# Performance work log

Hardware: AMD Instinct MI355X
Metric: run time of the kernel (lower is better)

The kernel has to match this reference:

```python
import jax, jax.numpy as jnp
import numpy as np

EPS = 1e-5
NEG_SLOPE = 0.01  # F.leaky_relu default


def setup_inputs() -> dict:
    key = jax.random.key(0)
    k1, k2, k3, k4 = jax.random.split(key, 4)
    N, F, H = 8192, 512, 2
    inputs = jax.random.normal(k1, (N, F), dtype=jnp.float32)
    adj = jnp.zeros((N, N), dtype=jnp.float32)  # accepted but unused by the module
    # torch Linear(F, F*H, bias=False): y = x @ W with W of shape [F, F*H]
    W = jax.random.normal(k2, (F, F * H), dtype=jnp.float32) * (1.0 / np.sqrt(F))
    a_w = jax.random.normal(k3, (1,), dtype=jnp.float32)  # Linear(1,1) weight
    a_b = jax.random.normal(k4, (1,), dtype=jnp.float32)  # Linear(1,1) bias
    return {"inputs": inputs, "adj": adj, "W": W, "a_w": a_w, "a_b": a_b}


def reference(inputs, adj, W, a_w, a_b):
    # Wh, Ws = chunk(inputs @ W, 2)
    WhWs = inputs @ W                       # [N, 2F]
    Wh, Ws = jnp.split(WhWs, 2, axis=-1)    # each [N, F]
    # bias = a(ones) = a_w * 1 + a_b  (constant scalar broadcast)
    bias = (a_w + a_b)[0]
    # dense attention: tanh(Wh + Ws + bias) @ Wh^T  -> [N, N]
    scores = jnp.tanh(Wh + Ws + bias) @ Wh.T
    attn = jax.nn.softmax(scores, axis=-1)  # [N, N]
    out = attn @ Wh + inputs                # [N, F] residual
    # training-mode batch norm over node dim, no affine
    mean = jnp.mean(out, axis=0)
    var = jnp.var(out, axis=0)
    out = (out - mean) * jax.lax.rsqrt(var + EPS)
    return jnp.where(out >= 0, out, NEG_SLOPE * out)
```

## Files before the change

### kernel.cpp

```cpp
#include <hip/hip_runtime.h>

using f32x4 = float    __attribute__((ext_vector_type(4)));
using f16x8 = _Float16 __attribute__((ext_vector_type(8)));

__device__ __forceinline__ void gload_lds16(const void* g, void* l) {
    __builtin_amdgcn_global_load_lds(
        (__attribute__((address_space(1))) void*)(void*)g,
        (__attribute__((address_space(3))) void*)l, 16, 0, 0);
}


__global__ __launch_bounds__(256) void k_cvt_x(
    const float* __restrict__ in, _Float16* __restrict__ out) {
    int i = (blockIdx.x * 256 + threadIdx.x) * 8;
    f32x4 a = *(const f32x4*)(in + i);
    f32x4 b = *(const f32x4*)(in + i + 4);
    f16x8 o;
    #pragma unroll
    for (int j = 0; j < 4; ++j) { o[j] = (_Float16)a[j]; o[j + 4] = (_Float16)b[j]; }
    *(f16x8*)(out + i) = o;
}

__global__ __launch_bounds__(256) void k_cvtT(
    const float* __restrict__ in, _Float16* __restrict__ out, int R, int C) {
    __shared__ _Float16 tile[32][33];
    int c0 = blockIdx.x * 32, r0 = blockIdx.y * 32;
    int tx = threadIdx.x & 31, ty = threadIdx.x >> 5;
    #pragma unroll
    for (int i = ty; i < 32; i += 8)
        tile[i][tx] = (_Float16)in[(size_t)(r0 + i) * C + c0 + tx];
    __syncthreads();
    #pragma unroll
    for (int i = ty; i < 32; i += 8)
        out[(size_t)(c0 + i) * R + r0 + tx] = tile[tx][i];
}

__global__ __launch_bounds__(256) void k_transpose16(
    const _Float16* __restrict__ in, _Float16* __restrict__ out, int R, int C) {
    __shared__ _Float16 tile[32][33];
    int c0 = blockIdx.x * 32, r0 = blockIdx.y * 32;
    int tx = threadIdx.x & 31, ty = threadIdx.x >> 5;
    #pragma unroll
    for (int i = ty; i < 32; i += 8)
        tile[i][tx] = in[(size_t)(r0 + i) * C + c0 + tx];
    __syncthreads();
    #pragma unroll
    for (int i = ty; i < 32; i += 8)
        out[(size_t)(c0 + i) * R + r0 + tx] = tile[tx][i];
}

template<int OM, int BN>
__global__ __launch_bounds__(256, 2) void k_gemm_bt(
    const _Float16* __restrict__ A, int lda,
    const _Float16* __restrict__ Bt, int ldb,
    void* __restrict__ Cp, int ldc, int K) {
    constexpr int BM  = 128;
    constexpr int NI  = BN / 32;
    constexpr int NCH = (BM + BN) / 16;
    __shared__ _Float16 As[BM * 32];
    __shared__ _Float16 Bs[BN * 32];
    const int row0 = blockIdx.y * BM, col0 = blockIdx.x * BN;
    const int tid = threadIdx.x, w = tid >> 6, lane = tid & 63;
    const int wm = w >> 1, wn = w & 1;
    const int lrow = lane & 15, quad = lane >> 4;
    const int r16 = lane >> 2;
    const int kc  = (((lane & 3) - ((lane >> 3) & 3)) & 3) * 8;
    const int sq  = ((quad + ((lrow >> 1) & 3)) & 3) * 8;
    f32x4 acc[4][NI] = {};

    for (int k0 = 0; k0 < K; k0 += 32) {
        #pragma unroll
        for (int i = 0; i < NCH / 4; ++i) {
            int c = w + i * 4;
            if (c < BM / 16) {
                gload_lds16(A + (size_t)(row0 + c * 16 + r16) * lda + (k0 + kc),
                            As + c * 512);
            } else {
                int c2 = c - BM / 16;
                gload_lds16(Bt + (size_t)(col0 + c2 * 16 + r16) * ldb + (k0 + kc),
                            Bs + c2 * 512);
            }
        }
        __syncthreads();
        f16x8 af[4], bfr[NI];
        #pragma unroll
        for (int i = 0; i < 4; ++i)
            af[i] = *(const f16x8*)(As + (wm * 64 + i * 16 + lrow) * 32 + sq);
        #pragma unroll
        for (int i = 0; i < NI; ++i)
            bfr[i] = *(const f16x8*)(Bs + (wn * (BN / 2) + i * 16 + lrow) * 32 + sq);
        #pragma unroll
        for (int mi = 0; mi < 4; ++mi)
            #pragma unroll
            for (int ni = 0; ni < NI; ++ni)
                acc[mi][ni] = __builtin_amdgcn_mfma_f32_16x16x32_f16(
                    af[mi], bfr[ni], acc[mi][ni], 0, 0, 0);
        __syncthreads();
    }
    #pragma unroll
    for (int mi = 0; mi < 4; ++mi) {
        #pragma unroll
        for (int ni = 0; ni < NI; ++ni) {
            int col = col0 + wn * (BN / 2) + ni * 16 + lrow;
            #pragma unroll
            for (int r = 0; r < 4; ++r) {
                int row = row0 + wm * 64 + mi * 16 + quad * 4 + r;
                float v = acc[mi][ni][r];
                if constexpr (OM == 1)
                    ((_Float16*)Cp)[(size_t)row * ldc + col] = (_Float16)v;
                else
                    ((float*)Cp)[(size_t)row * ldc + col] = v;
            }
        }
    }
}

__global__ __launch_bounds__(512, 4) void k_gemm3(
    const _Float16* __restrict__ A,
    const _Float16* __restrict__ Bt,
    float* __restrict__ Cp) {
    __shared__ _Float16 As[128 * 32];
    __shared__ _Float16 Bs[256 * 32];
    const int row0 = blockIdx.y * 128, col0 = blockIdx.x * 256;
    const size_t zoff = (size_t)blockIdx.z * 2048;
    Cp += (size_t)blockIdx.z * ((size_t)8192 * 512);
    const int tid = threadIdx.x, w = tid >> 6, lane = tid & 63;
    const int wm = w >> 2, wn = w & 3;
    const int lrow = lane & 15, quad = lane >> 4;
    const int r16 = lane >> 2;
    const int kc = (((lane & 3) - ((lane >> 3) & 3)) & 3) * 8;
    const int sq = ((quad + ((lrow >> 1) & 3)) & 3) * 8;
    f32x4 acc[4][4] = {};
    for (int k0 = 0; k0 < 2048; k0 += 32) {
        #pragma unroll
        for (int i = 0; i < 3; ++i) {
            int c = w + i * 8;
            if (c < 8) {
                gload_lds16(A + (size_t)(row0 + c * 16 + r16) * 8192 + zoff + k0 + kc,
                            As + c * 512);
            } else {
                int c2 = c - 8;
                gload_lds16(Bt + (size_t)(col0 + c2 * 16 + r16) * 8192 + zoff + k0 + kc,
                            Bs + c2 * 512);
            }
        }
        __syncthreads();
        f16x8 af[4], bf[4];
        #pragma unroll
        for (int i = 0; i < 4; ++i)
            af[i] = *(const f16x8*)(As + (wm * 64 + i * 16 + lrow) * 32 + sq);
        #pragma unroll
        for (int i = 0; i < 4; ++i)
            bf[i] = *(const f16x8*)(Bs + (wn * 64 + i * 16 + lrow) * 32 + sq);
        #pragma unroll
        for (int mi = 0; mi < 4; ++mi)
            #pragma unroll
            for (int ni = 0; ni < 4; ++ni)
                acc[mi][ni] = __builtin_amdgcn_mfma_f32_16x16x32_f16(
                    af[mi], bf[ni], acc[mi][ni], 0, 0, 0);
        __syncthreads();
    }
    #pragma unroll
    for (int mi = 0; mi < 4; ++mi) {
        #pragma unroll
        for (int ni = 0; ni < 4; ++ni) {
            int col = col0 + wn * 64 + ni * 16 + lrow;
            #pragma unroll
            for (int r = 0; r < 4; ++r) {
                int row = row0 + wm * 64 + mi * 16 + quad * 4 + r;
                Cp[(size_t)row * 512 + col] = acc[mi][ni][r];
            }
        }
    }
}

__global__ __launch_bounds__(256) void k_tanh_split(
    const float* __restrict__ WhWs, _Float16* __restrict__ T,
    _Float16* __restrict__ Wh,
    const float* __restrict__ aw, const float* __restrict__ ab) {
    int i = blockIdx.x * 256 + threadIdx.x;
    float bias = aw[0] + ab[0];
    int row = i >> 9, col = i & 511;
    float wh  = WhWs[(size_t)row * 1024 + col];
    float wsv = WhWs[(size_t)row * 1024 + 512 + col];
    Wh[i] = (_Float16)wh;
    T[i]  = (_Float16)tanhf(wh + wsv + bias);
}

__global__ __launch_bounds__(256) void k_softmax_rows(
    _Float16* __restrict__ S, int N) {
    const int row = blockIdx.x;
    _Float16* prow = S + (size_t)row * N;
    const int t = threadIdx.x;
    float v[32];
    #pragma unroll
    for (int it = 0; it < 4; ++it) {
        f16x8 h = *(const f16x8*)(prow + (it * 256 + t) * 8);
        #pragma unroll
        for (int j = 0; j < 8; ++j) v[it * 8 + j] = (float)h[j];
    }
    float m = v[0];
    #pragma unroll
    for (int j = 1; j < 32; ++j) m = fmaxf(m, v[j]);
    #pragma unroll
    for (int off = 32; off > 0; off >>= 1) m = fmaxf(m, __shfl_xor(m, off));
    __shared__ float red[8];
    const int wid = t >> 6, lane = t & 63;
    if (lane == 0) red[wid] = m;
    __syncthreads();
    m = fmaxf(fmaxf(red[0], red[1]), fmaxf(red[2], red[3]));
    float l = 0.f;
    #pragma unroll
    for (int j = 0; j < 32; ++j) l += __expf(v[j] - m);
    #pragma unroll
    for (int off = 32; off > 0; off >>= 1) l += __shfl_xor(l, off);
    if (lane == 0) red[4 + wid] = l;
    __syncthreads();
    float rl = 1.f / (red[4] + red[5] + red[6] + red[7]);
    #pragma unroll
    for (int it = 0; it < 4; ++it) {
        f16x8 pk;
        #pragma unroll
        for (int j = 0; j < 8; ++j)
            pk[j] = (_Float16)(__expf(v[it * 8 + j] - m) * rl);
        *(f16x8*)(prow + (it * 256 + t) * 8) = pk;
    }
}

__global__ __launch_bounds__(256) void k_reduce_stats(
    const float* __restrict__ part, const float* __restrict__ X,
    float* __restrict__ outf, float* __restrict__ cs, float* __restrict__ cq) {
    const int t = threadIdx.x;
    const int r0 = blockIdx.x * 32;
    constexpr size_t PS = (size_t)8192 * 512;
    float s0 = 0, q0 = 0, s1 = 0, q1 = 0;
    for (int r = 0; r < 32; ++r) {
        size_t base = (size_t)(r0 + r) * 512;
        float a = part[base + t] + part[PS + base + t]
                + part[2 * PS + base + t] + part[3 * PS + base + t] + X[base + t];
        float b = part[base + t + 256] + part[PS + base + t + 256]
                + part[2 * PS + base + t + 256] + part[3 * PS + base + t + 256]
                + X[base + t + 256];
        outf[base + t] = a;       outf[base + t + 256] = b;
        s0 += a; q0 += a * a; s1 += b; q1 += b * b;
    }
    atomicAdd(&cs[t], s0);       atomicAdd(&cq[t], q0);
    atomicAdd(&cs[t + 256], s1); atomicAdd(&cq[t + 256], q1);
}

__global__ __launch_bounds__(256) void k_bn_lrelu(
    const float* __restrict__ outf, const float* __restrict__ colsum,
    const float* __restrict__ colsq, float* __restrict__ out) {
    int i = blockIdx.x * 256 + threadIdx.x;
    int c = i & 511;
    constexpr float rN = 1.f / 8192.f;
    float mean = colsum[c] * rN;
    float var  = colsq[c] * rN - mean * mean;
    float y = (outf[i] - mean) * rsqrtf(var + 1e-5f);
    y = (y >= 0.f) ? y : 0.01f * y;
    out[i] = y;
}

extern "C" void kernel_launch(void* const* d_in, const int* in_sizes, int n_in,
                              void* d_out, int out_size, void* d_ws, size_t ws_size,
                              hipStream_t stream) {
    const float* X  = (const float*)d_in[0];
    const float* W  = (const float*)d_in[2];
    const float* aw = (const float*)d_in[3];
    const float* ab = (const float*)d_in[4];
    float* out = (float*)d_out;

    char* ws = (char*)d_ws;
    _Float16* Xh   = (_Float16*)(ws + 0x0);
    _Float16* Wt   = (_Float16*)(ws + 0x800000);
    float*    WhWs = (float*)   (ws + 0x900000);
    _Float16* T    = (_Float16*)(ws + 0x2900000);
    _Float16* Whh  = (_Float16*)(ws + 0x3100000);
    _Float16* WhT  = (_Float16*)(ws + 0x3900000);
    _Float16* S    = (_Float16*)(ws + 0x4100000);
    float*    outf = (float*)   (ws + 0xC100000);
    float*    part = (float*)   (ws + 0xD100000);
    float*    cs   = (float*)   (ws + 0x11100000);
    float*    cq   = (float*)   (ws + 0x11100800);

    hipMemsetAsync(cs, 0, 4096, stream);
    k_cvt_x<<<dim3((8192 * 512) / 2048), 256, 0, stream>>>(X, Xh);
    k_cvtT<<<dim3(1024 / 32, 512 / 32), 256, 0, stream>>>(W, Wt, 512, 1024);
    k_gemm_bt<0, 128><<<dim3(1024 / 128, 8192 / 128), 256, 0, stream>>>(
        Xh, 512, Wt, 512, WhWs, 1024, 512);
    k_tanh_split<<<dim3((8192 * 512) / 256), 256, 0, stream>>>(WhWs, T, Whh, aw, ab);
    k_transpose16<<<dim3(512 / 32, 8192 / 32), 256, 0, stream>>>(Whh, WhT, 8192, 512);
    k_gemm_bt<1, 128><<<dim3(8192 / 128, 8192 / 128), 256, 0, stream>>>(
        T, 512, Whh, 512, S, 8192, 512);
    k_softmax_rows<<<dim3(8192), 256, 0, stream>>>(S, 8192);
    k_gemm3<<<dim3(2, 64, 4), 512, 0, stream>>>(S, WhT, part);
    k_reduce_stats<<<dim3(256), 256, 0, stream>>>(part, X, outf, cs, cq);
    k_bn_lrelu<<<dim3((8192 * 512) / 256), 256, 0, stream>>>(outf, cs, cq, out);
}
```

Before: 565.8 us.

## Fuse tanh, split and transpose into first GEMM epilogue; enlarge score GEMM tile

The first GEMM now computes the matching Wh and Ws columns in the same block and applies tanh plus bias in its epilogue. It writes Wh, T and the transposed Wh directly, which removes the fp32 WhWs round trip, the tanh_split kernel and the transpose kernel. The score GEMM moves to a 256x128 tile with 512 threads, and softmax caches its exponentials instead of recomputing them. The risks are uncoalesced 8-byte strided stores to WhT and a different occupancy profile for the larger tile.

```diff
diff --git a/kernel.cpp b/kernel.cpp
--- a/kernel.cpp
+++ b/kernel.cpp
@@ -2,6 +2,7 @@
 
 using f32x4 = float    __attribute__((ext_vector_type(4)));
 using f16x8 = _Float16 __attribute__((ext_vector_type(8)));
+using f16x4 = _Float16 __attribute__((ext_vector_type(4)));
 
 __device__ __forceinline__ void gload_lds16(const void* g, void* l) {
     __builtin_amdgcn_global_load_lds(
@@ -35,81 +36,115 @@
         out[(size_t)(c0 + i) * R + r0 + tx] = tile[tx][i];
 }
 
-__global__ __launch_bounds__(256) void k_transpose16(
-    const _Float16* __restrict__ in, _Float16* __restrict__ out, int R, int C) {
-    __shared__ _Float16 tile[32][33];
-    int c0 = blockIdx.x * 32, r0 = blockIdx.y * 32;
-    int tx = threadIdx.x & 31, ty = threadIdx.x >> 5;
-    #pragma unroll
-    for (int i = ty; i < 32; i += 8)
-        tile[i][tx] = in[(size_t)(r0 + i) * C + c0 + tx];
-    __syncthreads();
-    #pragma unroll
-    for (int i = ty; i < 32; i += 8)
-        out[(size_t)(c0 + i) * R + r0 + tx] = tile[tx][i];
-}
-
-template<int OM, int BN>
-__global__ __launch_bounds__(256, 2) void k_gemm_bt(
-    const _Float16* __restrict__ A, int lda,
-    const _Float16* __restrict__ Bt, int ldb,
-    void* __restrict__ Cp, int ldc, int K) {
-    constexpr int BM  = 128;
-    constexpr int NI  = BN / 32;
-    constexpr int NCH = (BM + BN) / 16;
-    __shared__ _Float16 As[BM * 32];
-    __shared__ _Float16 Bs[BN * 32];
-    const int row0 = blockIdx.y * BM, col0 = blockIdx.x * BN;
+__global__ __launch_bounds__(512, 4) void k_gemm1f(
+    const _Float16* __restrict__ A, const _Float16* __restrict__ Bt,
+    _Float16* __restrict__ Whh, _Float16* __restrict__ T,
+    _Float16* __restrict__ WhT,
+    const float* __restrict__ aw, const float* __restrict__ ab) {
+    __shared__ _Float16 As[128 * 32];
+    __shared__ _Float16 B0s[64 * 32];
+    __shared__ _Float16 B1s[64 * 32];
+    const float bias = aw[0] + ab[0];
+    const int row0 = blockIdx.y * 128, col0 = blockIdx.x * 64;
+    const int tid = threadIdx.x, w = tid >> 6, lane = tid & 63;
+    const int wm = w >> 2, wn = w & 3;
+    const int lrow = lane & 15, quad = lane >> 4;
+    const int r16 = lane >> 2;
+    const int kc = (((lane & 3) - ((lane >> 3) & 3)) & 3) * 8;
+    const int sq = ((quad + ((lrow >> 1) & 3)) & 3) * 8;
+    f32x4 acc0[4] = {}, acc1[4] = {};
+    for (int k0 = 0; k0 < 512; k0 += 32) {
+        gload_lds16(A + (size_t)(row0 + w * 16 + r16) * 512 + k0 + kc,
+                    As + w * 512);
+        if (w < 4)
+            gload_lds16(Bt + (size_t)(col0 + w * 16 + r16) * 512 + k0 + kc,
+                        B0s + w * 512);
+        else
+            gload_lds16(Bt + (size_t)(col0 + 512 + (w - 4) * 16 + r16) * 512 + k0 + kc,
+                        B1s + (w - 4) * 512);
+        __syncthreads();
+        f16x8 af[4], b0, b1;
+        #pragma unroll
+        for (int i = 0; i < 4; ++i)
+            af[i] = *(const f16x8*)(As + (wm * 64 + i * 16 + lrow) * 32 + sq);
+        b0 = *(const f16x8*)(B0s + (wn * 16 + lrow) * 32 + sq);
+        b1 = *(const f16x8*)(B1s + (wn * 16 + lrow) * 32 + sq);
+        #pragma unroll
+        for (int mi = 0; mi < 4; ++mi) {
+            acc0[mi] = __builtin_amdgcn_mfma_f32_16x16x32_f16(af[mi], b0, acc0[mi], 0, 0, 0);
+            acc1[mi] = __builtin_amdgcn_mfma_f32_16x16x32_f16(af[mi], b1, acc1[mi], 0, 0, 0);
+        }
+        __syncthreads();
+    }
+    const int col = col0 + wn * 16 + lrow;
+    #pragma unroll
+    for (int mi = 0; mi < 4; ++mi) {
+        int rowb = row0 + wm * 64 + mi * 16 + quad * 4;
+        f16x4 pw;
+        #pragma unroll
+        for (int r = 0; r < 4; ++r) {
+            float wh = acc0[mi][r];
+            float tt = tanhf(wh + acc1[mi][r] + bias);
+            Whh[(size_t)(rowb + r) * 512 + col] = (_Float16)wh;
+            T[(size_t)(rowb + r) * 512 + col]   = (_Float16)tt;
+            pw[r] = (_Float16)wh;
+        }
+        *(f16x4*)(WhT + (size_t)col * 8192 + rowb) = pw;
+    }
+}
+
+__global__ __launch_bounds__(512, 4) void k_gemm2(
+    const _Float16* __restrict__ A,
+    const _Float16* __restrict__ Bt,
+    _Float16* __restrict__ Cp) {
+    __shared__ _Float16 As[256 * 32];
+    __shared__ _Float16 Bs[128 * 32];
+    const int row0 = blockIdx.y * 256, col0 = blockIdx.x * 128;
     const int tid = threadIdx.x, w = tid >> 6, lane = tid & 63;
     const int wm = w >> 1, wn = w & 1;
     const int lrow = lane & 15, quad = lane >> 4;
     const int r16 = lane >> 2;
-    const int kc  = (((lane & 3) - ((lane >> 3) & 3)) & 3) * 8;
-    const int sq  = ((quad + ((lrow >> 1) & 3)) & 3) * 8;
-    f32x4 acc[4][NI] = {};
-
-    for (int k0 = 0; k0 < K; k0 += 32) {
-        #pragma unroll
-        for (int i = 0; i < NCH / 4; ++i) {
-            int c = w + i * 4;
-            if (c < BM / 16) {
-                gload_lds16(A + (size_t)(row0 + c * 16 + r16) * lda + (k0 + kc),
+    const int kc = (((lane & 3) - ((lane >> 3) & 3)) & 3) * 8;
+    const int sq = ((quad + ((lrow >> 1) & 3)) & 3) * 8;
+    f32x4 acc[4][4] = {};
+    for (int k0 = 0; k0 < 512; k0 += 32) {
+        #pragma unroll
+        for (int i = 0; i < 3; ++i) {
+            int c = w + i * 8;
+            if (c < 16) {
+                gload_lds16(A + (size_t)(row0 + c * 16 + r16) * 512 + k0 + kc,
                             As + c * 512);
             } else {
-                int c2 = c - BM / 16;
-                gload_lds16(Bt + (size_t)(col0 + c2 * 16 + r16) * ldb + (k0 + kc),
+                int c2 = c - 16;
+                gload_lds16(Bt + (size_t)(col0 + c2 * 16 + r16) * 512 + k0 + kc,
                             Bs + c2 * 512);
             }
         }
         __syncthreads();
-        f16x8 af[4], bfr[NI];
+        f16x8 af[4], bf[4];
         #pragma unroll
         for (int i = 0; i < 4; ++i)
             af[i] = *(const f16x8*)(As + (wm * 64 + i * 16 + lrow) * 32 + sq);
         #pragma unroll
-        for (int i = 0; i < NI; ++i)
-            bfr[i] = *(const f16x8*)(Bs + (wn * (BN / 2) + i * 16 + lrow) * 32 + sq);
+        for (int i = 0; i < 4; ++i)
+            bf[i] = *(const f16x8*)(Bs + (wn * 64 + i * 16 + lrow) * 32 + sq);
         #pragma unroll
         for (int mi = 0; mi < 4; ++mi)
             #pragma unroll
-            for (int ni = 0; ni < NI; ++ni)
+            for (int ni = 0; ni < 4; ++ni)
                 acc[mi][ni] = __builtin_amdgcn_mfma_f32_16x16x32_f16(
-                    af[mi], bfr[ni], acc[mi][ni], 0, 0, 0);
+                    af[mi], bf[ni], acc[mi][ni], 0, 0, 0);
         __syncthreads();
     }
     #pragma unroll
     for (int mi = 0; mi < 4; ++mi) {
         #pragma unroll
-        for (int ni = 0; ni < NI; ++ni) {
-            int col = col0 + wn * (BN / 2) + ni * 16 + lrow;
+        for (int ni = 0; ni < 4; ++ni) {
+            int col = col0 + wn * 64 + ni * 16 + lrow;
             #pragma unroll
             for (int r = 0; r < 4; ++r) {
                 int row = row0 + wm * 64 + mi * 16 + quad * 4 + r;
-                float v = acc[mi][ni][r];
-                if constexpr (OM == 1)
-                    ((_Float16*)Cp)[(size_t)row * ldc + col] = (_Float16)v;
-                else
-                    ((float*)Cp)[(size_t)row * ldc + col] = v;
+                Cp[(size_t)row * 8192 + col] = (_Float16)acc[mi][ni][r];
             }
         }
     }
@@ -174,19 +209,6 @@
     }
 }
 
-__global__ __launch_bounds__(256) void k_tanh_split(
-    const float* __restrict__ WhWs, _Float16* __restrict__ T,
-    _Float16* __restrict__ Wh,
-    const float* __restrict__ aw, const float* __restrict__ ab) {
-    int i = blockIdx.x * 256 + threadIdx.x;
-    float bias = aw[0] + ab[0];
-    int row = i >> 9, col = i & 511;
-    float wh  = WhWs[(size_t)row * 1024 + col];
-    float wsv = WhWs[(size_t)row * 1024 + 512 + col];
-    Wh[i] = (_Float16)wh;
-    T[i]  = (_Float16)tanhf(wh + wsv + bias);
-}
-
 __global__ __launch_bounds__(256) void k_softmax_rows(
     _Float16* __restrict__ S, int N) {
     const int row = blockIdx.x;
@@ -211,7 +233,7 @@
     m = fmaxf(fmaxf(red[0], red[1]), fmaxf(red[2], red[3]));
     float l = 0.f;
     #pragma unroll
-    for (int j = 0; j < 32; ++j) l += __expf(v[j] - m);
+    for (int j = 0; j < 32; ++j) { v[j] = __expf(v[j] - m); l += v[j]; }
     #pragma unroll
     for (int off = 32; off > 0; off >>= 1) l += __shfl_xor(l, off);
     if (lane == 0) red[4 + wid] = l;
@@ -222,7 +244,7 @@
         f16x8 pk;
         #pragma unroll
         for (int j = 0; j < 8; ++j)
-            pk[j] = (_Float16)(__expf(v[it * 8 + j] - m) * rl);
+            pk[j] = (_Float16)(v[it * 8 + j] * rl);
         *(f16x8*)(prow + (it * 256 + t) * 8) = pk;
     }
 }
@@ -273,25 +295,20 @@
     char* ws = (char*)d_ws;
     _Float16* Xh   = (_Float16*)(ws + 0x0);
     _Float16* Wt   = (_Float16*)(ws + 0x800000);
-    float*    WhWs = (float*)   (ws + 0x900000);
-    _Float16* T    = (_Float16*)(ws + 0x2900000);
-    _Float16* Whh  = (_Float16*)(ws + 0x3100000);
-    _Float16* WhT  = (_Float16*)(ws + 0x3900000);
-    _Float16* S    = (_Float16*)(ws + 0x4100000);
-    float*    outf = (float*)   (ws + 0xC100000);
-    float*    part = (float*)   (ws + 0xD100000);
-    float*    cs   = (float*)   (ws + 0x11100000);
-    float*    cq   = (float*)   (ws + 0x11100800);
+    _Float16* T    = (_Float16*)(ws + 0x900000);
+    _Float16* Whh  = (_Float16*)(ws + 0x1100000);
+    _Float16* WhT  = (_Float16*)(ws + 0x1900000);
+    _Float16* S    = (_Float16*)(ws + 0x2100000);
+    float*    outf = (float*)   (ws + 0xA100000);
+    float*    part = (float*)   (ws + 0xB100000);
+    float*    cs   = (float*)   (ws + 0xF100000);
+    float*    cq   = (float*)   (ws + 0xF100800);
 
     hipMemsetAsync(cs, 0, 4096, stream);
     k_cvt_x<<<dim3((8192 * 512) / 2048), 256, 0, stream>>>(X, Xh);
     k_cvtT<<<dim3(1024 / 32, 512 / 32), 256, 0, stream>>>(W, Wt, 512, 1024);
-    k_gemm_bt<0, 128><<<dim3(1024 / 128, 8192 / 128), 256, 0, stream>>>(
-        Xh, 512, Wt, 512, WhWs, 1024, 512);
-    k_tanh_split<<<dim3((8192 * 512) / 256), 256, 0, stream>>>(WhWs, T, Whh, aw, ab);
-    k_transpose16<<<dim3(512 / 32, 8192 / 32), 256, 0, stream>>>(Whh, WhT, 8192, 512);
-    k_gemm_bt<1, 128><<<dim3(8192 / 128, 8192 / 128), 256, 0, stream>>>(
-        T, 512, Whh, 512, S, 8192, 512);
+    k_gemm1f<<<dim3(8, 64), 512, 0, stream>>>(Xh, Wt, Whh, T, WhT, aw, ab);
+    k_gemm2<<<dim3(64, 32), 512, 0, stream>>>(T, Whh, S);
     k_softmax_rows<<<dim3(8192), 256, 0, stream>>>(S, 8192);
     k_gemm3<<<dim3(2, 64, 4), 512, 0, stream>>>(S, WhT, part);
     k_reduce_stats<<<dim3(256), 256, 0, stream>>>(part, X, outf, cs, cq);
```

Result: faster. 544.8 us (-3.7%).
